# Performance work log

Measured on AMD Instinct MI355X. Metric: run time of the kernel, lower is better.

The kernel has to match this reference:

```python
import jax, jax.numpy as jnp
import numpy as np

LN_EPS = 1e-5
ADJ_EPS = 1e-8
LRELU_SLOPE = 0.2


def _layernorm(x, g, b):
    m = x.mean(-1, keepdims=True)
    v = ((x - m) ** 2).mean(-1, keepdims=True)
    return (x - m) / jnp.sqrt(v + LN_EPS) * g + b


def _gat(h, adj, W, a, dim_head, proj=None):
    # h: [B,N,Din]; adj: [B,N,N]; W: [Din, H*dh]; a: [H, 2*dh]
    B, N, _ = h.shape
    H = a.shape[0]
    ht = (h @ W).reshape(B, N, H, dim_head)          # [B,N,H,dh]
    # additive attention: a . [h_i || h_j] splits into two rank-1 terms,
    # so we never materialize the O(B N^2 H 2dh) concat tensor.
    ei = jnp.einsum('bnhd,hd->bnh', ht, a[:, :dim_head])
    ej = jnp.einsum('bnhd,hd->bnh', ht, a[:, dim_head:])
    e = ei[:, :, None, :] + ej[:, None, :, :]        # [B,N,N,H]
    e = jnp.where(e > 0, e, LRELU_SLOPE * e)         # leaky relu(0.2)
    mask = (adj > 0)[..., None]                      # [B,N,N,1]
    e = jnp.where(mask, e, -jnp.inf)
    alpha = jax.nn.softmax(e, axis=2)                # softmax over neighbors m
    hagg = jnp.einsum('bnmh,bmhd->bnhd', alpha, ht)  # [B,N,H,dh]
    out = hagg.reshape(B, N, -1)
    if proj is not None:
        Wp, bp = proj
        out = out @ Wp + bp
    return out


def setup_inputs() -> dict:
    key = jax.random.key(0)
    ks = jax.random.split(key, 24)
    B, N, DN, DH, H = 64, 360, 360, 256, 8
    s = 0.05
    nrm = lambda k, sh, sc=s: (jax.random.normal(k, sh) * sc).astype(jnp.float32)
    return {
        'mind_matrix': jax.random.uniform(ks[0], (B, N, N), dtype=jnp.float32),
        'roi_features_img': jax.random.normal(ks[1], (B, N, DH), dtype=jnp.float32),
        'group_prior': jax.random.uniform(ks[2], (N, N), dtype=jnp.float32),
        'Wnp': nrm(ks[3], (DN, DH)), 'bnp': jnp.zeros((DH,), jnp.float32),
        'Wrf': nrm(ks[4], (2 * DH, DH)), 'brf': jnp.zeros((DH,), jnp.float32),
        'ln_g': jnp.ones((DH,), jnp.float32), 'ln_b': jnp.zeros((DH,), jnp.float32),
        'Wp1': nrm(ks[5], (1, 32)), 'bp1': jnp.zeros((32,), jnp.float32),
        'Wp2': nrm(ks[6], (32, 1)), 'bp2': jnp.zeros((1,), jnp.float32),
        'gatW0': nrm(ks[7], (DH, DH)), 'gata0': nrm(ks[8], (H, 64), 1.0),
        'gatW1': nrm(ks[9], (DH, DH)), 'gata1': nrm(ks[10], (H, 64), 1.0),
        'gatW2': nrm(ks[11], (DH, H * DH)), 'gata2': nrm(ks[12], (H, 2 * DH), 1.0),
        'projW': nrm(ks[13], (H * DH, DH)), 'projb': jnp.zeros((DH,), jnp.float32),
        'Wr1': nrm(ks[14], (DH, DH)), 'br1': jnp.zeros((DH,), jnp.float32),
        'Wr2': nrm(ks[15], (DH, DH)), 'br2': jnp.zeros((DH,), jnp.float32),
    }


def reference(mind_matrix, roi_features_img, group_prior,
              Wnp, bnp, Wrf, brf, ln_g, ln_b,
              Wp1, bp1, Wp2, bp2,
              gatW0, gata0, gatW1, gata1, gatW2, gata2, projW, projb,
              Wr1, br1, Wr2, br2):
    # node feature fusion
    node_mind = mind_matrix @ Wnp + bnp                       # [B,N,256]
    nf = jnp.concatenate([node_mind, roi_features_img], -1) @ Wrf + brf
    nf = jax.nn.gelu(_layernorm(nf, ln_g, ln_b), approximate=False)
    # prior-modulated adjacency (tau = 1.0)
    adj_base = jnp.exp(-mind_matrix)                          # [B,N,N]
    pm = jax.nn.relu(group_prior[..., None] @ Wp1 + bp1)      # [N,N,32]
    pm = jax.nn.sigmoid(pm @ Wp2 + bp2)[..., 0]               # [N,N]
    adj_mod = adj_base * (1.0 + pm)[None]
    adj_norm = adj_mod / (adj_mod.sum(-1, keepdims=True) + ADJ_EPS)
    # hierarchical GAT (dropout inactive at eval)
    h = _gat(nf, adj_norm, gatW0, gata0, 32)
    h = _gat(h, adj_norm, gatW1, gata1, 32)
    h = _gat(h, adj_norm, gatW2, gata2, 256, (projW, projb))  # concat=False layer
    # attention readout
    node_attention = jax.nn.softmax(jnp.linalg.norm(h, axis=-1), axis=-1)  # [B,N]
    ge = jnp.einsum('bn,bnd->bd', node_attention, h)
    ge = jax.nn.gelu(ge @ Wr1 + br1, approximate=False) @ Wr2 + br2
    return ge, h, node_attention
```

## Files before the change

kernel.cpp:

```cpp
#include <hip/hip_runtime.h>
#include <hip/hip_bf16.h>
#include <math.h>


#define B_ 64
#define N_ 360
#define D_ 256
#define H_ 8
#define ROWS_ (B_ * N_)

__device__ __forceinline__ float gelu_f(float x) {
    return 0.5f * x * (1.f + erff(x * 0.70710678118654752440f));
}

__global__ __launch_bounds__(256) void gemm_tiled(
    const float* __restrict__ A1, const float* __restrict__ B1, int K1, int lda1, int ldb1,
    const float* __restrict__ A2, const float* __restrict__ B2, int K2, int lda2, int ldb2,
    const float* __restrict__ bias, float* __restrict__ C, int M, int N, int ldc,
    size_t sA, size_t sB, size_t sC)
{
    __shared__ float As[2][32][132];
    __shared__ float Bs[2][32][64];
    const int tid = threadIdx.x;
    const int z = blockIdx.z;
    const int bm = blockIdx.y * 128;
    const int bn = blockIdx.x * 64;
    const int tr = (tid >> 4) * 8;
    const int tc = (tid & 15) * 4;
    const int lar = tid >> 3;
    const int lak = (tid & 7) * 4;
    const int lbk = tid >> 4;
    const int lbc = (tid & 15) * 4;

    float acc[8][4] = {};
    float4 rA[4], rB[2];

    for (int pass = 0; pass < 2; ++pass) {
        const float* Ab = pass ? A2 : A1;
        const float* Bb = pass ? B2 : B1;
        if (Ab == nullptr) continue;
        const float* A  = Ab + (pass ? (size_t)0 : (size_t)z * sA);
        const float* Bm = Bb + (pass ? (size_t)0 : (size_t)z * sB);
        const int K   = pass ? K2 : K1;
        const int lda = pass ? lda2 : lda1;
        const int ldb = pass ? ldb2 : ldb1;
        const int S = (K + 31) >> 5;

        auto loadA = [&](int s) {
            const int k0 = s << 5;
            #pragma unroll
            for (int j = 0; j < 4; ++j) {
                const int gr = bm + lar + j * 32;
                const int gk = k0 + lak;
                float4 v; v.x = v.y = v.z = v.w = 0.f;
                if (gr < M) {
                    if (gk + 3 < K) {
                        v = *(const float4*)&A[(size_t)gr * lda + gk];
                    } else {
                        float t0 = 0.f, t1 = 0.f, t2 = 0.f, t3 = 0.f;
                        if (gk + 0 < K) t0 = A[(size_t)gr * lda + gk + 0];
                        if (gk + 1 < K) t1 = A[(size_t)gr * lda + gk + 1];
                        if (gk + 2 < K) t2 = A[(size_t)gr * lda + gk + 2];
                        if (gk + 3 < K) t3 = A[(size_t)gr * lda + gk + 3];
                        v.x = t0; v.y = t1; v.z = t2; v.w = t3;
                    }
                }
                rA[j] = v;
            }
        };
        auto loadB = [&](int s) {
            const int k0 = s << 5;
            #pragma unroll
            for (int j = 0; j < 2; ++j) {
                const int gk = k0 + lbk + j * 16;
                float4 v; v.x = v.y = v.z = v.w = 0.f;
                if (gk < K) v = *(const float4*)&Bm[(size_t)gk * ldb + bn + lbc];
                rB[j] = v;
            }
        };
        auto storeA = [&](int buf) {
            #pragma unroll
            for (int j = 0; j < 4; ++j) {
                const int row = lar + j * 32;
                As[buf][lak + 0][row] = rA[j].x;
                As[buf][lak + 1][row] = rA[j].y;
                As[buf][lak + 2][row] = rA[j].z;
                As[buf][lak + 3][row] = rA[j].w;
            }
        };
        auto storeB = [&](int buf) {
            #pragma unroll
            for (int j = 0; j < 2; ++j)
                *(float4*)&Bs[buf][lbk + j * 16][lbc] = rB[j];
        };

        loadA(0); loadB(0);
        storeA(0); storeB(0);
        __syncthreads();
        for (int s = 0; s < S; ++s) {
            const int cur = s & 1;
            if (s + 1 < S) { loadA(s + 1); loadB(s + 1); }
            #pragma unroll
            for (int k = 0; k < 32; ++k) {
                const float4 a0 = *(const float4*)&As[cur][k][tr];
                const float4 a1 = *(const float4*)&As[cur][k][tr + 4];
                const float4 bv = *(const float4*)&Bs[cur][k][tc];
                const float av[8] = {a0.x, a0.y, a0.z, a0.w, a1.x, a1.y, a1.z, a1.w};
                const float bb[4] = {bv.x, bv.y, bv.z, bv.w};
                #pragma unroll
                for (int i = 0; i < 8; ++i)
                    #pragma unroll
                    for (int j = 0; j < 4; ++j)
                        acc[i][j] += av[i] * bb[j];
            }
            if (s + 1 < S) { storeA(cur ^ 1); storeB(cur ^ 1); }
            __syncthreads();
        }
    }

    float4 bz; bz.x = bz.y = bz.z = bz.w = 0.f;
    if (bias) bz = *(const float4*)&bias[bn + tc];
    float* Cz = C + (size_t)z * sC;
    #pragma unroll
    for (int i = 0; i < 8; ++i) {
        const int r = bm + tr + i;
        if (r < M) {
            float4 o;
            o.x = acc[i][0] + bz.x;
            o.y = acc[i][1] + bz.y;
            o.z = acc[i][2] + bz.z;
            o.w = acc[i][3] + bz.w;
            *(float4*)&Cz[(size_t)r * ldc + bn + tc] = o;
        }
    }
}

__global__ __launch_bounds__(256) void biascomb_kernel(
    const float* __restrict__ bnp, const float* __restrict__ Wrf,
    const float* __restrict__ brf, float* __restrict__ bcomb)
{
    int c = threadIdx.x;
    float acc = brf[c];
    for (int k = 0; k < 256; ++k) acc += bnp[k] * Wrf[k * 256 + c];
    bcomb[c] = acc;
}

__global__ __launch_bounds__(256) void uv_kernel(
    const float* __restrict__ gatW2, const float* __restrict__ a2,
    float* __restrict__ u, float* __restrict__ v)
{
    const int h = blockIdx.x;
    const int i = threadIdx.x;
    const float* wrow = gatW2 + (size_t)i * 2048 + h * 256;
    const float* ai = a2 + h * 512;
    float su = 0.f, sv = 0.f;
    for (int j = 0; j < 256; ++j) {
        float w = wrow[j];
        su += w * ai[j];
        sv += w * ai[256 + j];
    }
    u[h * 256 + i] = su;
    v[h * 256 + i] = sv;
}

__global__ __launch_bounds__(64) void ln_gelu_kernel(
    float* __restrict__ x, const float* __restrict__ g, const float* __restrict__ b)
{
    const size_t row = blockIdx.x;
    const int t = threadIdx.x;
    float4 v = *(const float4*)&x[row * 256 + t * 4];
    float s = v.x + v.y + v.z + v.w;
    #pragma unroll
    for (int m = 1; m < 64; m <<= 1) s += __shfl_xor(s, m);
    float mean = s * (1.f / 256.f);
    float dx = v.x - mean, dy = v.y - mean, dz = v.z - mean, dw = v.w - mean;
    float q = dx * dx + dy * dy + dz * dz + dw * dw;
    #pragma unroll
    for (int m = 1; m < 64; m <<= 1) q += __shfl_xor(q, m);
    float rstd = 1.f / sqrtf(q * (1.f / 256.f) + 1e-5f);
    float4 gg = *(const float4*)&g[t * 4];
    float4 bb = *(const float4*)&b[t * 4];
    float4 r;
    r.x = gelu_f(dx * rstd * gg.x + bb.x);
    r.y = gelu_f(dy * rstd * gg.y + bb.y);
    r.z = gelu_f(dz * rstd * gg.z + bb.z);
    r.w = gelu_f(dw * rstd * gg.w + bb.w);
    *(float4*)&x[row * 256 + t * 4] = r;
}

template <int DH>
__global__ __launch_bounds__(64) void eiej_kernel(
    const float* __restrict__ ht, const float* __restrict__ a,
    float* __restrict__ ei, float* __restrict__ ej)
{
    const size_t row = blockIdx.x;
    const int t = threadIdx.x;
    constexpr int E = (H_ * DH) / 64;
    const int h = t >> 3;
    const int d0 = (t & 7) * E;
    const float* hp = ht + row * (H_ * DH) + h * DH + d0;
    const float* ap = a + h * 2 * DH + d0;
    float se = 0.f, sj = 0.f;
    #pragma unroll
    for (int i = 0; i < E; i += 4) {
        float4 x = *(const float4*)&hp[i];
        float4 u = *(const float4*)&ap[i];
        float4 w = *(const float4*)&ap[DH + i];
        se += x.x * u.x + x.y * u.y + x.z * u.z + x.w * u.w;
        sj += x.x * w.x + x.y * w.y + x.z * w.z + x.w * w.w;
    }
    se += __shfl_xor(se, 1); sj += __shfl_xor(sj, 1);
    se += __shfl_xor(se, 2); sj += __shfl_xor(sj, 2);
    se += __shfl_xor(se, 4); sj += __shfl_xor(sj, 4);
    if ((t & 7) == 0) {
        ei[row * H_ + h] = se;
        ej[row * H_ + h] = sj;
    }
}

__global__ __launch_bounds__(64) void eiej2_kernel(
    const float* __restrict__ h2, const float* __restrict__ u,
    const float* __restrict__ v, float* __restrict__ ei, float* __restrict__ ej)
{
    const size_t row = blockIdx.x;
    const int t = threadIdx.x;
    const int h = t >> 3;
    const int d0 = (t & 7) * 32;
    const float* hp = h2 + row * 256 + d0;
    const float* up = u + h * 256 + d0;
    const float* vp = v + h * 256 + d0;
    float se = 0.f, sj = 0.f;
    #pragma unroll
    for (int i = 0; i < 32; i += 4) {
        float4 x = *(const float4*)&hp[i];
        float4 uu = *(const float4*)&up[i];
        float4 vv = *(const float4*)&vp[i];
        se += x.x * uu.x + x.y * uu.y + x.z * uu.z + x.w * uu.w;
        sj += x.x * vv.x + x.y * vv.y + x.z * vv.z + x.w * vv.w;
    }
    se += __shfl_xor(se, 1); sj += __shfl_xor(sj, 1);
    se += __shfl_xor(se, 2); sj += __shfl_xor(sj, 2);
    se += __shfl_xor(se, 4); sj += __shfl_xor(sj, 4);
    if ((t & 7) == 0) {
        ei[row * H_ + h] = se;
        ej[row * H_ + h] = sj;
    }
}

__global__ __launch_bounds__(256) void gat_agg32(
    const float* __restrict__ ht, const float* __restrict__ ei,
    const float* __restrict__ ej, float* __restrict__ out)
{
    __shared__ float scT[N_][32];
    __shared__ float ejs[N_];
    __shared__ float eis[32];
    __shared__ float psum[8][32];
    __shared__ float rinv_s[32];
    __shared__ float red4[4];
    const int tid = threadIdx.x;
    const int bh = blockIdx.y;
    const int b = bh >> 3, h = bh & 7;
    const int n0 = blockIdx.x * 32;
    const int nrows = min(32, N_ - n0);

    for (int m = tid; m < N_; m += 256) ejs[m] = ej[(b * N_ + m) * H_ + h];
    if (tid < 32) eis[tid] = (tid < nrows) ? ei[(size_t)(b * N_ + n0 + tid) * H_ + h] : 0.f;
    __syncthreads();

    float mx = -1e30f;
    for (int m = tid; m < N_; m += 256) mx = fmaxf(mx, ejs[m]);
    #pragma unroll
    for (int s = 1; s < 64; s <<= 1) mx = fmaxf(mx, __shfl_xor(mx, s));
    if ((tid & 63) == 0) red4[tid >> 6] = mx;
    __syncthreads();
    const float maxej = fmaxf(fmaxf(red4[0], red4[1]), fmaxf(red4[2], red4[3]));

    {
        const int r = tid & 31, sub = tid >> 5;
        const float ei_r = eis[r];
        float mrow = ei_r + maxej;
        mrow = mrow > 0.f ? mrow : 0.2f * mrow;
        float s = 0.f;
        for (int m = sub; m < N_; m += 8) {
            float e = ei_r + ejs[m];
            e = e > 0.f ? e : 0.2f * e;
            float p = __expf(e - mrow);
            scT[m][r] = p;
            s += p;
        }
        psum[sub][r] = s;
    }
    __syncthreads();
    if (tid < 32) {
        float s = psum[0][tid] + psum[1][tid] + psum[2][tid] + psum[3][tid]
                + psum[4][tid] + psum[5][tid] + psum[6][tid] + psum[7][tid];
        rinv_s[tid] = 1.f / s;
    }
    __syncthreads();

    const int mq = tid >> 6;
    const int rg = (tid >> 3) & 7;
    const int cg = tid & 7;
    const float* Vp = ht + (size_t)b * N_ * D_ + h * 32 + cg * 4;
    float acc[4][4] = {};
    for (int m = mq; m < N_; m += 4) {
        const float4 a4 = *(const float4*)&scT[m][rg * 4];
        const float4 v4 = *(const float4*)&Vp[(size_t)m * D_];
        const float a[4] = {a4.x, a4.y, a4.z, a4.w};
        const float v[4] = {v4.x, v4.y, v4.z, v4.w};
        #pragma unroll
        for (int i = 0; i < 4; ++i)
            #pragma unroll
            for (int j = 0; j < 4; ++j)
                acc[i][j] += a[i] * v[j];
    }
    __syncthreads();

    float* red = &scT[0][0];
    {
        float* rp = red + mq * 1088 + (rg * 8 + cg) * 17;
        #pragma unroll
        for (int i = 0; i < 4; ++i)
            #pragma unroll
            for (int j = 0; j < 4; ++j)
                rp[i * 4 + j] = acc[i][j];
    }
    __syncthreads();
    for (int o = tid; o < 1024; o += 256) {
        const int lane = o >> 4, k = o & 15;
        const float v = red[0 * 1088 + lane * 17 + k] + red[1 * 1088 + lane * 17 + k]
                      + red[2 * 1088 + lane * 17 + k] + red[3 * 1088 + lane * 17 + k];
        const int rgg = lane >> 3, cgg = lane & 7, i = k >> 2, j = k & 3;
        const int r = rgg * 4 + i, c = cgg * 4 + j;
        if (r < nrows)
            out[(size_t)(b * N_ + n0 + r) * D_ + h * 32 + c] = v * rinv_s[r];
    }
}

__global__ __launch_bounds__(256) void gat2_agg(
    const float* __restrict__ Z, const float* __restrict__ ei,
    const float* __restrict__ ej, const float* __restrict__ projb,
    float* __restrict__ out, int h)
{
    __shared__ float scT[N_][32];
    __shared__ float ejs[N_];
    __shared__ float eis[32];
    __shared__ float psum[8][32];
    __shared__ float rinv_s[32];
    __shared__ float red4[4];
    const int tid = threadIdx.x;
    const int b = blockIdx.y;
    const int n0 = blockIdx.x * 32;
    const int nrows = min(32, N_ - n0);

    for (int m = tid; m < N_; m += 256) ejs[m] = ej[(b * N_ + m) * H_ + h];
    if (tid < 32) eis[tid] = (tid < nrows) ? ei[(size_t)(b * N_ + n0 + tid) * H_ + h] : 0.f;
    __syncthreads();

    float mx = -1e30f;
    for (int m = tid; m < N_; m += 256) mx = fmaxf(mx, ejs[m]);
    #pragma unroll
    for (int s = 1; s < 64; s <<= 1) mx = fmaxf(mx, __shfl_xor(mx, s));
    if ((tid & 63) == 0) red4[tid >> 6] = mx;
    __syncthreads();
    const float maxej = fmaxf(fmaxf(red4[0], red4[1]), fmaxf(red4[2], red4[3]));

    {
        const int r = tid & 31, sub = tid >> 5;
        const float ei_r = eis[r];
        float mrow = ei_r + maxej;
        mrow = mrow > 0.f ? mrow : 0.2f * mrow;
        float s = 0.f;
        for (int m = sub; m < N_; m += 8) {
            float e = ei_r + ejs[m];
            e = e > 0.f ? e : 0.2f * e;
            float p = __expf(e - mrow);
            scT[m][r] = p;
            s += p;
        }
        psum[sub][r] = s;
    }
    __syncthreads();
    if (tid < 32) {
        float s = psum[0][tid] + psum[1][tid] + psum[2][tid] + psum[3][tid]
                + psum[4][tid] + psum[5][tid] + psum[6][tid] + psum[7][tid];
        rinv_s[tid] = 1.f / s;
    }
    __syncthreads();

    const int rg = tid >> 5;
    const int cg = tid & 31;
    const float* Vp = Z + (size_t)b * N_ * D_ + cg * 8;
    float acc[4][8] = {};
    #pragma unroll 2
    for (int m = 0; m < N_; ++m) {
        const float4 a4 = *(const float4*)&scT[m][rg * 4];
        const float4 v0 = *(const float4*)&Vp[(size_t)m * D_];
        const float4 v1 = *(const float4*)&Vp[(size_t)m * D_ + 4];
        const float a[4] = {a4.x, a4.y, a4.z, a4.w};
        const float v[8] = {v0.x, v0.y, v0.z, v0.w, v1.x, v1.y, v1.z, v1.w};
        #pragma unroll
        for (int i = 0; i < 4; ++i)
            #pragma unroll
            for (int j = 0; j < 8; ++j)
                acc[i][j] += a[i] * v[j];
    }

    #pragma unroll
    for (int i = 0; i < 4; ++i) {
        const int r = rg * 4 + i;
        if (r < nrows) {
            const float ri = rinv_s[r];
            float* op = out + (size_t)(b * N_ + n0 + r) * D_ + cg * 8;
            if (h == 0) {
                const float4 p0 = *(const float4*)&projb[cg * 8];
                const float4 p1 = *(const float4*)&projb[cg * 8 + 4];
                float4 o0, o1;
                o0.x = acc[i][0] * ri + p0.x; o0.y = acc[i][1] * ri + p0.y;
                o0.z = acc[i][2] * ri + p0.z; o0.w = acc[i][3] * ri + p0.w;
                o1.x = acc[i][4] * ri + p1.x; o1.y = acc[i][5] * ri + p1.y;
                o1.z = acc[i][6] * ri + p1.z; o1.w = acc[i][7] * ri + p1.w;
                *(float4*)&op[0] = o0;
                *(float4*)&op[4] = o1;
            } else {
                float4 o0 = *(const float4*)&op[0];
                float4 o1 = *(const float4*)&op[4];
                o0.x += acc[i][0] * ri; o0.y += acc[i][1] * ri;
                o0.z += acc[i][2] * ri; o0.w += acc[i][3] * ri;
                o1.x += acc[i][4] * ri; o1.y += acc[i][5] * ri;
                o1.z += acc[i][6] * ri; o1.w += acc[i][7] * ri;
                *(float4*)&op[0] = o0;
                *(float4*)&op[4] = o1;
            }
        }
    }
}

__global__ __launch_bounds__(64) void rownorm_kernel(
    const float* __restrict__ h, float* __restrict__ nrm)
{
    const size_t row = blockIdx.x;
    const int t = threadIdx.x;
    float4 v = *(const float4*)&h[row * 256 + t * 4];
    float s = v.x * v.x + v.y * v.y + v.z * v.z + v.w * v.w;
    #pragma unroll
    for (int m = 1; m < 64; m <<= 1) s += __shfl_xor(s, m);
    if (t == 0) nrm[row] = sqrtf(s);
}

__global__ __launch_bounds__(64) void softmax_n_kernel(
    const float* __restrict__ nrm, float* __restrict__ attn)
{
    const int b = blockIdx.x;
    const int t = threadIdx.x;
    float v[6];
    float mx = -1e30f;
    #pragma unroll
    for (int i = 0; i < 6; ++i) {
        int m = t + i * 64;
        v[i] = (m < N_) ? nrm[b * N_ + m] : -1e30f;
        mx = fmaxf(mx, v[i]);
    }
    #pragma unroll
    for (int m = 1; m < 64; m <<= 1) mx = fmaxf(mx, __shfl_xor(mx, m));
    float s = 0.f;
    #pragma unroll
    for (int i = 0; i < 6; ++i) {
        int m = t + i * 64;
        float p = (m < N_) ? __expf(v[i] - mx) : 0.f;
        v[i] = p;
        s += p;
    }
    #pragma unroll
    for (int m = 1; m < 64; m <<= 1) s += __shfl_xor(s, m);
    const float inv = 1.f / s;
    #pragma unroll
    for (int i = 0; i < 6; ++i) {
        int m = t + i * 64;
        if (m < N_) attn[b * N_ + m] = v[i] * inv;
    }
}

__global__ __launch_bounds__(256) void ge_kernel(
    const float* __restrict__ attn, const float* __restrict__ h, float* __restrict__ ge)
{
    __shared__ float a[N_];
    const int b = blockIdx.x;
    const int t = threadIdx.x;
    for (int m = t; m < N_; m += 256) a[m] = attn[b * N_ + m];
    __syncthreads();
    float acc = 0.f;
    const float* hp = h + (size_t)b * N_ * 256 + t;
    for (int m = 0; m < N_; ++m) acc += a[m] * hp[(size_t)m * 256];
    ge[b * 256 + t] = acc;
}

__global__ __launch_bounds__(256) void mlp_kernel(
    const float* __restrict__ X, const float* __restrict__ W,
    const float* __restrict__ bias, float* __restrict__ Y, int applyGelu)
{
    __shared__ float xs[256];
    const int b = blockIdx.x;
    const int t = threadIdx.x;
    xs[t] = X[b * 256 + t];
    __syncthreads();
    float acc = bias[t];
    for (int k = 0; k < 256; ++k) acc += xs[k] * W[k * 256 + t];
    if (applyGelu) acc = gelu_f(acc);
    Y[b * 256 + t] = acc;
}


extern "C" void kernel_launch(void* const* d_in, const int* in_sizes, int n_in,
                              void* d_out, int out_size, void* d_ws, size_t ws_size,
                              hipStream_t stream) {
    const float* mind  = (const float*)d_in[0];
    const float* roi   = (const float*)d_in[1];
    const float* Wnp   = (const float*)d_in[3];
    const float* bnp   = (const float*)d_in[4];
    const float* Wrf   = (const float*)d_in[5];
    const float* brf   = (const float*)d_in[6];
    const float* ln_g  = (const float*)d_in[7];
    const float* ln_b  = (const float*)d_in[8];
    const float* gatW0 = (const float*)d_in[13];
    const float* gata0 = (const float*)d_in[14];
    const float* gatW1 = (const float*)d_in[15];
    const float* gata1 = (const float*)d_in[16];
    const float* gatW2 = (const float*)d_in[17];
    const float* gata2 = (const float*)d_in[18];
    const float* projW = (const float*)d_in[19];
    const float* projb = (const float*)d_in[20];
    const float* Wr1   = (const float*)d_in[21];
    const float* br1   = (const float*)d_in[22];
    const float* Wr2   = (const float*)d_in[23];
    const float* br2   = (const float*)d_in[24];

    const size_t SZ = (size_t)ROWS_ * D_;
    float* ws    = (float*)d_ws;
    float* nf    = ws;
    float* h1    = nf + SZ;
    float* h2    = h1 + SZ;
    float* ht01  = h2 + SZ;
    float* Z     = ht01 + SZ;
    float* ei_b  = Z + SZ;
    float* ej_b  = ei_b + ROWS_ * H_;
    float* Wcomb = ej_b + ROWS_ * H_;
    float* bcomb = Wcomb + 360 * 256;
    float* Gbuf  = bcomb + 256;
    float* uvec  = Gbuf + 8 * 256 * 256;
    float* vvec  = uvec + 8 * 256;
    float* norms = vvec + 8 * 256;
    float* ge0   = norms + ROWS_;
    float* ge1   = ge0 + B_ * D_;

    const size_t need = (size_t)(ge1 + B_ * D_ - ws) * sizeof(float);
    if (ws_size < need) return;

    float* out    = (float*)d_out;
    float* out_ge = out;
    float* out_h  = out + (size_t)B_ * D_;
    float* out_at = out_h + (size_t)ROWS_ * D_;

    const dim3 blk(256);

    gemm_tiled<<<dim3(4, 3), blk, 0, stream>>>(
        Wnp, Wrf, 256, 256, 256,
        nullptr, nullptr, 0, 0, 0,
        nullptr, Wcomb, 360, 256, 256, 0, 0, 0);
    biascomb_kernel<<<1, 256, 0, stream>>>(bnp, Wrf, brf, bcomb);
    gemm_tiled<<<dim3(4, 180), blk, 0, stream>>>(
        mind, Wcomb, 360, 360, 256,
        roi, Wrf + 256 * 256, 256, 256, 256,
        bcomb, nf, ROWS_, 256, 256, 0, 0, 0);
    ln_gelu_kernel<<<ROWS_, 64, 0, stream>>>(nf, ln_g, ln_b);

    gemm_tiled<<<dim3(4, 180), blk, 0, stream>>>(
        nf, gatW0, 256, 256, 256,
        nullptr, nullptr, 0, 0, 0,
        nullptr, ht01, ROWS_, 256, 256, 0, 0, 0);
    eiej_kernel<32><<<ROWS_, 64, 0, stream>>>(ht01, gata0, ei_b, ej_b);
    gat_agg32<<<dim3(12, B_ * H_), blk, 0, stream>>>(ht01, ei_b, ej_b, h1);

    gemm_tiled<<<dim3(4, 180), blk, 0, stream>>>(
        h1, gatW1, 256, 256, 256,
        nullptr, nullptr, 0, 0, 0,
        nullptr, ht01, ROWS_, 256, 256, 0, 0, 0);
    eiej_kernel<32><<<ROWS_, 64, 0, stream>>>(ht01, gata1, ei_b, ej_b);
    gat_agg32<<<dim3(12, B_ * H_), blk, 0, stream>>>(ht01, ei_b, ej_b, h2);

    gemm_tiled<<<dim3(4, 2, 8), blk, 0, stream>>>(
        gatW2, projW, 256, 2048, 256,
        nullptr, nullptr, 0, 0, 0,
        nullptr, Gbuf, 256, 256, 256,
        256, (size_t)256 * 256, (size_t)256 * 256);
    uv_kernel<<<8, 256, 0, stream>>>(gatW2, gata2, uvec, vvec);
    eiej2_kernel<<<ROWS_, 64, 0, stream>>>(h2, uvec, vvec, ei_b, ej_b);

    for (int h = 0; h < H_; ++h) {
        gemm_tiled<<<dim3(4, 180), blk, 0, stream>>>(
            h2, Gbuf + (size_t)h * 256 * 256, 256, 256, 256,
            nullptr, nullptr, 0, 0, 0,
            nullptr, Z, ROWS_, 256, 256, 0, 0, 0);
        gat2_agg<<<dim3(12, B_), blk, 0, stream>>>(
            Z, ei_b, ej_b, projb, out_h, h);
    }

    rownorm_kernel<<<ROWS_, 64, 0, stream>>>(out_h, norms);
    softmax_n_kernel<<<B_, 64, 0, stream>>>(norms, out_at);
    ge_kernel<<<B_, 256, 0, stream>>>(out_at, out_h, ge0);
    mlp_kernel<<<B_, 256, 0, stream>>>(ge0, Wr1, br1, ge1, 1);
    mlp_kernel<<<B_, 256, 0, stream>>>(ge1, Wr2, br2, out_ge, 0);
}
```

Baseline: 2.408 ms.

## Fuse all heads per GAT block and batch final-layer heads four at a time

Rewrites the layer-0/1 aggregation so one block handles all 8 heads for a 32-row tile. Softmax scores are computed in chunks of 30 neighbors and consumed immediately, and the block writes full 256-wide rows with vectorized stores instead of reducing partials across four wavefront groups. The final GAT layer now launches batched GEMMs (grid z=4) producing four head projections at once. A gat2_agg4 kernel then accumulates four heads in registers, cutting launches and read-modify-write passes over out_h from 8 to 2. This costs more shared memory, more per-chunk barriers, and a second exp pass per head in the final-layer kernel.

```diff
diff --git a/kernel.cpp b/kernel.cpp
--- a/kernel.cpp
+++ b/kernel.cpp
@@ -8,6 +8,8 @@
 #define D_ 256
 #define H_ 8
 #define ROWS_ (B_ * N_)
+#define CHUNK01 30
+#define SCPAD 964
 
 __device__ __forceinline__ float gelu_f(float x) {
     return 0.5f * x * (1.f + erff(x * 0.70710678118654752440f));
@@ -247,100 +249,104 @@
     }
 }
 
-__global__ __launch_bounds__(256) void gat_agg32(
+__global__ __launch_bounds__(256) void gat01_agg(
     const float* __restrict__ ht, const float* __restrict__ ei,
     const float* __restrict__ ej, float* __restrict__ out)
 {
-    __shared__ float scT[N_][32];
-    __shared__ float ejs[N_];
-    __shared__ float eis[32];
-    __shared__ float psum[8][32];
-    __shared__ float rinv_s[32];
-    __shared__ float red4[4];
+    __shared__ float scT[8 * SCPAD];
+    __shared__ float ejs[8][N_];
+    __shared__ float eis[8][32];
+    __shared__ float rinv_s[8][32];
+    __shared__ float maxej_s[8];
     const int tid = threadIdx.x;
-    const int bh = blockIdx.y;
-    const int b = bh >> 3, h = bh & 7;
+    const int b = blockIdx.y;
     const int n0 = blockIdx.x * 32;
     const int nrows = min(32, N_ - n0);
 
-    for (int m = tid; m < N_; m += 256) ejs[m] = ej[(b * N_ + m) * H_ + h];
-    if (tid < 32) eis[tid] = (tid < nrows) ? ei[(size_t)(b * N_ + n0 + tid) * H_ + h] : 0.f;
+    for (int idx = tid; idx < N_ * H_; idx += 256) {
+        const int m = idx >> 3, h = idx & 7;
+        ejs[h][m] = ej[(size_t)(b * N_ + m) * H_ + h];
+    }
+    const int ph = tid >> 5, pr = tid & 31;
+    eis[ph][pr] = (pr < nrows) ? ei[(size_t)(b * N_ + n0 + pr) * H_ + ph] : 0.f;
     __syncthreads();
 
-    float mx = -1e30f;
-    for (int m = tid; m < N_; m += 256) mx = fmaxf(mx, ejs[m]);
-    #pragma unroll
-    for (int s = 1; s < 64; s <<= 1) mx = fmaxf(mx, __shfl_xor(mx, s));
-    if ((tid & 63) == 0) red4[tid >> 6] = mx;
+    {
+        float mx = -1e30f;
+        for (int m = pr; m < N_; m += 32) mx = fmaxf(mx, ejs[ph][m]);
+        mx = fmaxf(mx, __shfl_xor(mx, 1));
+        mx = fmaxf(mx, __shfl_xor(mx, 2));
+        mx = fmaxf(mx, __shfl_xor(mx, 4));
+        mx = fmaxf(mx, __shfl_xor(mx, 8));
+        mx = fmaxf(mx, __shfl_xor(mx, 16));
+        if (pr == 0) maxej_s[ph] = mx;
+    }
     __syncthreads();
-    const float maxej = fmaxf(fmaxf(red4[0], red4[1]), fmaxf(red4[2], red4[3]));
-
-    {
-        const int r = tid & 31, sub = tid >> 5;
-        const float ei_r = eis[r];
-        float mrow = ei_r + maxej;
-        mrow = mrow > 0.f ? mrow : 0.2f * mrow;
-        float s = 0.f;
-        for (int m = sub; m < N_; m += 8) {
-            float e = ei_r + ejs[m];
+
+    const float ei_r = eis[ph][pr];
+    float mrow = ei_r + maxej_s[ph];
+    mrow = mrow > 0.f ? mrow : 0.2f * mrow;
+    float rsum = 0.f;
+
+    const int rg = tid >> 5, cg = tid & 31;
+    const int vh = cg >> 2;
+    const float* Vp = ht + (size_t)b * N_ * D_ + cg * 8;
+    float acc[4][8] = {};
+
+    for (int c0 = 0; c0 < N_; c0 += CHUNK01) {
+        float* sp = scT + ph * SCPAD + pr;
+        #pragma unroll 6
+        for (int mm = 0; mm < CHUNK01; ++mm) {
+            float e = ei_r + ejs[ph][c0 + mm];
             e = e > 0.f ? e : 0.2f * e;
             float p = __expf(e - mrow);
-            scT[m][r] = p;
-            s += p;
-        }
-        psum[sub][r] = s;
-    }
+            sp[mm * 32] = p;
+            rsum += p;
+        }
+        __syncthreads();
+        const float* st = scT + vh * SCPAD + rg * 4;
+        #pragma unroll 2
+        for (int mm = 0; mm < CHUNK01; ++mm) {
+            const int m = c0 + mm;
+            const float4 a4 = *(const float4*)&st[mm * 32];
+            const float4 v0 = *(const float4*)&Vp[(size_t)m * D_];
+            const float4 v1 = *(const float4*)&Vp[(size_t)m * D_ + 4];
+            const float a[4] = {a4.x, a4.y, a4.z, a4.w};
+            const float v[8] = {v0.x, v0.y, v0.z, v0.w, v1.x, v1.y, v1.z, v1.w};
+            #pragma unroll
+            for (int i = 0; i < 4; ++i)
+                #pragma unroll
+                for (int j = 0; j < 8; ++j)
+                    acc[i][j] += a[i] * v[j];
+        }
+        __syncthreads();
+    }
+
+    rinv_s[ph][pr] = 1.f / rsum;
     __syncthreads();
-    if (tid < 32) {
-        float s = psum[0][tid] + psum[1][tid] + psum[2][tid] + psum[3][tid]
-                + psum[4][tid] + psum[5][tid] + psum[6][tid] + psum[7][tid];
-        rinv_s[tid] = 1.f / s;
-    }
-    __syncthreads();
-
-    const int mq = tid >> 6;
-    const int rg = (tid >> 3) & 7;
-    const int cg = tid & 7;
-    const float* Vp = ht + (size_t)b * N_ * D_ + h * 32 + cg * 4;
-    float acc[4][4] = {};
-    for (int m = mq; m < N_; m += 4) {
-        const float4 a4 = *(const float4*)&scT[m][rg * 4];
-        const float4 v4 = *(const float4*)&Vp[(size_t)m * D_];
-        const float a[4] = {a4.x, a4.y, a4.z, a4.w};
-        const float v[4] = {v4.x, v4.y, v4.z, v4.w};
-        #pragma unroll
-        for (int i = 0; i < 4; ++i)
-            #pragma unroll
-            for (int j = 0; j < 4; ++j)
-                acc[i][j] += a[i] * v[j];
-    }
-    __syncthreads();
-
-    float* red = &scT[0][0];
-    {
-        float* rp = red + mq * 1088 + (rg * 8 + cg) * 17;
-        #pragma unroll
-        for (int i = 0; i < 4; ++i)
-            #pragma unroll
-            for (int j = 0; j < 4; ++j)
-                rp[i * 4 + j] = acc[i][j];
-    }
-    __syncthreads();
-    for (int o = tid; o < 1024; o += 256) {
-        const int lane = o >> 4, k = o & 15;
-        const float v = red[0 * 1088 + lane * 17 + k] + red[1 * 1088 + lane * 17 + k]
-                      + red[2 * 1088 + lane * 17 + k] + red[3 * 1088 + lane * 17 + k];
-        const int rgg = lane >> 3, cgg = lane & 7, i = k >> 2, j = k & 3;
-        const int r = rgg * 4 + i, c = cgg * 4 + j;
-        if (r < nrows)
-            out[(size_t)(b * N_ + n0 + r) * D_ + h * 32 + c] = v * rinv_s[r];
-    }
-}
-
-__global__ __launch_bounds__(256) void gat2_agg(
-    const float* __restrict__ Z, const float* __restrict__ ei,
-    const float* __restrict__ ej, const float* __restrict__ projb,
-    float* __restrict__ out, int h)
+
+    #pragma unroll
+    for (int i = 0; i < 4; ++i) {
+        const int r = rg * 4 + i;
+        if (r < nrows) {
+            const float ri = rinv_s[vh][r];
+            float* op = out + (size_t)(b * N_ + n0 + r) * D_ + cg * 8;
+            float4 o0, o1;
+            o0.x = acc[i][0] * ri; o0.y = acc[i][1] * ri;
+            o0.z = acc[i][2] * ri; o0.w = acc[i][3] * ri;
+            o1.x = acc[i][4] * ri; o1.y = acc[i][5] * ri;
+            o1.z = acc[i][6] * ri; o1.w = acc[i][7] * ri;
+            *(float4*)&op[0] = o0;
+            *(float4*)&op[4] = o1;
+        }
+    }
+}
+
+__global__ __launch_bounds__(256) void gat2_agg4(
+    const float* __restrict__ Zbase, size_t zstride,
+    const float* __restrict__ ei, const float* __restrict__ ej,
+    const float* __restrict__ projb, float* __restrict__ out,
+    int hbase, int first)
 {
     __shared__ float scT[N_][32];
     __shared__ float ejs[N_];
@@ -352,83 +358,89 @@
     const int b = blockIdx.y;
     const int n0 = blockIdx.x * 32;
     const int nrows = min(32, N_ - n0);
-
-    for (int m = tid; m < N_; m += 256) ejs[m] = ej[(b * N_ + m) * H_ + h];
-    if (tid < 32) eis[tid] = (tid < nrows) ? ei[(size_t)(b * N_ + n0 + tid) * H_ + h] : 0.f;
-    __syncthreads();
-
-    float mx = -1e30f;
-    for (int m = tid; m < N_; m += 256) mx = fmaxf(mx, ejs[m]);
-    #pragma unroll
-    for (int s = 1; s < 64; s <<= 1) mx = fmaxf(mx, __shfl_xor(mx, s));
-    if ((tid & 63) == 0) red4[tid >> 6] = mx;
-    __syncthreads();
-    const float maxej = fmaxf(fmaxf(red4[0], red4[1]), fmaxf(red4[2], red4[3]));
-
-    {
-        const int r = tid & 31, sub = tid >> 5;
-        const float ei_r = eis[r];
+    const int rg = tid >> 5, cg = tid & 31;
+    const int sr = tid & 31, sub = tid >> 5;
+    float acc[4][8] = {};
+
+    for (int hh = 0; hh < 4; ++hh) {
+        const int h = hbase + hh;
+        for (int m = tid; m < N_; m += 256) ejs[m] = ej[(size_t)(b * N_ + m) * H_ + h];
+        if (tid < 32) eis[tid] = (tid < nrows) ? ei[(size_t)(b * N_ + n0 + tid) * H_ + h] : 0.f;
+        __syncthreads();
+
+        float mx = -1e30f;
+        for (int m = tid; m < N_; m += 256) mx = fmaxf(mx, ejs[m]);
+        #pragma unroll
+        for (int s = 1; s < 64; s <<= 1) mx = fmaxf(mx, __shfl_xor(mx, s));
+        if ((tid & 63) == 0) red4[tid >> 6] = mx;
+        __syncthreads();
+        const float maxej = fmaxf(fmaxf(red4[0], red4[1]), fmaxf(red4[2], red4[3]));
+
+        const float ei_r = eis[sr];
         float mrow = ei_r + maxej;
         mrow = mrow > 0.f ? mrow : 0.2f * mrow;
+
         float s = 0.f;
         for (int m = sub; m < N_; m += 8) {
             float e = ei_r + ejs[m];
             e = e > 0.f ? e : 0.2f * e;
-            float p = __expf(e - mrow);
-            scT[m][r] = p;
-            s += p;
-        }
-        psum[sub][r] = s;
-    }
-    __syncthreads();
-    if (tid < 32) {
-        float s = psum[0][tid] + psum[1][tid] + psum[2][tid] + psum[3][tid]
-                + psum[4][tid] + psum[5][tid] + psum[6][tid] + psum[7][tid];
-        rinv_s[tid] = 1.f / s;
-    }
-    __syncthreads();
-
-    const int rg = tid >> 5;
-    const int cg = tid & 31;
-    const float* Vp = Z + (size_t)b * N_ * D_ + cg * 8;
-    float acc[4][8] = {};
-    #pragma unroll 2
-    for (int m = 0; m < N_; ++m) {
-        const float4 a4 = *(const float4*)&scT[m][rg * 4];
-        const float4 v0 = *(const float4*)&Vp[(size_t)m * D_];
-        const float4 v1 = *(const float4*)&Vp[(size_t)m * D_ + 4];
-        const float a[4] = {a4.x, a4.y, a4.z, a4.w};
-        const float v[8] = {v0.x, v0.y, v0.z, v0.w, v1.x, v1.y, v1.z, v1.w};
-        #pragma unroll
-        for (int i = 0; i < 4; ++i)
+            s += __expf(e - mrow);
+        }
+        psum[sub][sr] = s;
+        __syncthreads();
+        if (tid < 32) {
+            float t = psum[0][tid] + psum[1][tid] + psum[2][tid] + psum[3][tid]
+                    + psum[4][tid] + psum[5][tid] + psum[6][tid] + psum[7][tid];
+            rinv_s[tid] = 1.f / t;
+        }
+        __syncthreads();
+        const float ri = rinv_s[sr];
+        for (int m = sub; m < N_; m += 8) {
+            float e = ei_r + ejs[m];
+            e = e > 0.f ? e : 0.2f * e;
+            scT[m][sr] = __expf(e - mrow) * ri;
+        }
+        __syncthreads();
+
+        const float* Vp = Zbase + (size_t)hh * zstride + (size_t)b * N_ * D_ + cg * 8;
+        #pragma unroll 2
+        for (int m = 0; m < N_; ++m) {
+            const float4 a4 = *(const float4*)&scT[m][rg * 4];
+            const float4 v0 = *(const float4*)&Vp[(size_t)m * D_];
+            const float4 v1 = *(const float4*)&Vp[(size_t)m * D_ + 4];
+            const float a[4] = {a4.x, a4.y, a4.z, a4.w};
+            const float v[8] = {v0.x, v0.y, v0.z, v0.w, v1.x, v1.y, v1.z, v1.w};
             #pragma unroll
-            for (int j = 0; j < 8; ++j)
-                acc[i][j] += a[i] * v[j];
+            for (int i = 0; i < 4; ++i)
+                #pragma unroll
+                for (int j = 0; j < 8; ++j)
+                    acc[i][j] += a[i] * v[j];
+        }
+        __syncthreads();
     }
 
     #pragma unroll
     for (int i = 0; i < 4; ++i) {
         const int r = rg * 4 + i;
         if (r < nrows) {
-            const float ri = rinv_s[r];
             float* op = out + (size_t)(b * N_ + n0 + r) * D_ + cg * 8;
-            if (h == 0) {
+            if (first) {
                 const float4 p0 = *(const float4*)&projb[cg * 8];
                 const float4 p1 = *(const float4*)&projb[cg * 8 + 4];
                 float4 o0, o1;
-                o0.x = acc[i][0] * ri + p0.x; o0.y = acc[i][1] * ri + p0.y;
-                o0.z = acc[i][2] * ri + p0.z; o0.w = acc[i][3] * ri + p0.w;
-                o1.x = acc[i][4] * ri + p1.x; o1.y = acc[i][5] * ri + p1.y;
-                o1.z = acc[i][6] * ri + p1.z; o1.w = acc[i][7] * ri + p1.w;
+                o0.x = acc[i][0] + p0.x; o0.y = acc[i][1] + p0.y;
+                o0.z = acc[i][2] + p0.z; o0.w = acc[i][3] + p0.w;
+                o1.x = acc[i][4] + p1.x; o1.y = acc[i][5] + p1.y;
+                o1.z = acc[i][6] + p1.z; o1.w = acc[i][7] + p1.w;
                 *(float4*)&op[0] = o0;
                 *(float4*)&op[4] = o1;
             } else {
                 float4 o0 = *(const float4*)&op[0];
                 float4 o1 = *(const float4*)&op[4];
-                o0.x += acc[i][0] * ri; o0.y += acc[i][1] * ri;
-                o0.z += acc[i][2] * ri; o0.w += acc[i][3] * ri;
-                o1.x += acc[i][4] * ri; o1.y += acc[i][5] * ri;
-                o1.z += acc[i][6] * ri; o1.w += acc[i][7] * ri;
+                o0.x += acc[i][0]; o0.y += acc[i][1];
+                o0.z += acc[i][2]; o0.w += acc[i][3];
+                o1.x += acc[i][4]; o1.y += acc[i][5];
+                o1.z += acc[i][6]; o1.w += acc[i][7];
                 *(float4*)&op[0] = o0;
                 *(float4*)&op[4] = o1;
             }
@@ -536,15 +548,16 @@
     const float* br2   = (const float*)d_in[24];
 
     const size_t SZ = (size_t)ROWS_ * D_;
-    float* ws    = (float*)d_ws;
-    float* nf    = ws;
-    float* h1    = nf + SZ;
-    float* h2    = h1 + SZ;
-    float* ht01  = h2 + SZ;
-    float* Z     = ht01 + SZ;
-    float* ei_b  = Z + SZ;
-    float* ej_b  = ei_b + ROWS_ * H_;
-    float* Wcomb = ej_b + ROWS_ * H_;
+    float* ws = (float*)d_ws;
+    float* s0 = ws;
+    float* s1 = ws + SZ;
+    float* s2 = ws + 2 * SZ;
+    float* s3 = ws + 3 * SZ;
+    float* s4 = ws + 4 * SZ;
+    float* tail  = ws + 5 * SZ;
+    float* ei_b  = tail;
+    float* ej_b  = ei_b + (size_t)ROWS_ * H_;
+    float* Wcomb = ej_b + (size_t)ROWS_ * H_;
     float* bcomb = Wcomb + 360 * 256;
     float* Gbuf  = bcomb + 256;
     float* uvec  = Gbuf + 8 * 256 * 256;
@@ -571,22 +584,22 @@
     gemm_tiled<<<dim3(4, 180), blk, 0, stream>>>(
         mind, Wcomb, 360, 360, 256,
         roi, Wrf + 256 * 256, 256, 256, 256,
-        bcomb, nf, ROWS_, 256, 256, 0, 0, 0);
-    ln_gelu_kernel<<<ROWS_, 64, 0, stream>>>(nf, ln_g, ln_b);
+        bcomb, s1, ROWS_, 256, 256, 0, 0, 0);
+    ln_gelu_kernel<<<ROWS_, 64, 0, stream>>>(s1, ln_g, ln_b);
 
     gemm_tiled<<<dim3(4, 180), blk, 0, stream>>>(
-        nf, gatW0, 256, 256, 256,
+        s1, gatW0, 256, 256, 256,
         nullptr, nullptr, 0, 0, 0,
-        nullptr, ht01, ROWS_, 256, 256, 0, 0, 0);
-    eiej_kernel<32><<<ROWS_, 64, 0, stream>>>(ht01, gata0, ei_b, ej_b);
-    gat_agg32<<<dim3(12, B_ * H_), blk, 0, stream>>>(ht01, ei_b, ej_b, h1);
+        nullptr, s2, ROWS_, 256, 256, 0, 0, 0);
+    eiej_kernel<32><<<ROWS_, 64, 0, stream>>>(s2, gata0, ei_b, ej_b);
+    gat01_agg<<<dim3(12, B_), blk, 0, stream>>>(s2, ei_b, ej_b, s3);
 
     gemm_tiled<<<dim3(4, 180), blk, 0, stream>>>(
-        h1, gatW1, 256, 256, 256,
+        s3, gatW1, 256, 256, 256,
         nullptr, nullptr, 0, 0, 0,
-        nullptr, ht01, ROWS_, 256, 256, 0, 0, 0);
-    eiej_kernel<32><<<ROWS_, 64, 0, stream>>>(ht01, gata1, ei_b, ej_b);
-    gat_agg32<<<dim3(12, B_ * H_), blk, 0, stream>>>(ht01, ei_b, ej_b, h2);
+        nullptr, s2, ROWS_, 256, 256, 0, 0, 0);
+    eiej_kernel<32><<<ROWS_, 64, 0, stream>>>(s2, gata1, ei_b, ej_b);
+    gat01_agg<<<dim3(12, B_), blk, 0, stream>>>(s2, ei_b, ej_b, s0);
 
     gemm_tiled<<<dim3(4, 2, 8), blk, 0, stream>>>(
         gatW2, projW, 256, 2048, 256,
@@ -594,16 +607,22 @@
         nullptr, Gbuf, 256, 256, 256,
         256, (size_t)256 * 256, (size_t)256 * 256);
     uv_kernel<<<8, 256, 0, stream>>>(gatW2, gata2, uvec, vvec);
-    eiej2_kernel<<<ROWS_, 64, 0, stream>>>(h2, uvec, vvec, ei_b, ej_b);
-
-    for (int h = 0; h < H_; ++h) {
-        gemm_tiled<<<dim3(4, 180), blk, 0, stream>>>(
-            h2, Gbuf + (size_t)h * 256 * 256, 256, 256, 256,
-            nullptr, nullptr, 0, 0, 0,
-            nullptr, Z, ROWS_, 256, 256, 0, 0, 0);
-        gat2_agg<<<dim3(12, B_), blk, 0, stream>>>(
-            Z, ei_b, ej_b, projb, out_h, h);
-    }
+    eiej2_kernel<<<ROWS_, 64, 0, stream>>>(s0, uvec, vvec, ei_b, ej_b);
+
+    gemm_tiled<<<dim3(4, 180, 4), blk, 0, stream>>>(
+        s0, Gbuf, 256, 256, 256,
+        nullptr, nullptr, 0, 0, 0,
+        nullptr, s1, ROWS_, 256, 256,
+        0, (size_t)256 * 256, SZ);
+    gat2_agg4<<<dim3(12, B_), blk, 0, stream>>>(
+        s1, SZ, ei_b, ej_b, projb, out_h, 0, 1);
+    gemm_tiled<<<dim3(4, 180, 4), blk, 0, stream>>>(
+        s0, Gbuf + (size_t)4 * 256 * 256, 256, 256, 256,
+        nullptr, nullptr, 0, 0, 0,
+        nullptr, s1, ROWS_, 256, 256,
+        0, (size_t)256 * 256, SZ);
+    gat2_agg4<<<dim3(12, B_), blk, 0, stream>>>(
+        s1, SZ, ei_b, ej_b, projb, out_h, 4, 0);
 
     rownorm_kernel<<<ROWS_, 64, 0, stream>>>(out_h, norms);
     softmax_n_kernel<<<B_, 64, 0, stream>>>(norms, out_at);
```

Result: faster. 2.048 ms (-15.0%).
